# Kernel optimization log

Measured on AMD Instinct MI355X. Metric: run time of the kernel, lower is better.

The kernel has to match this reference:

```python
import jax, jax.numpy as jnp
import numpy as np

B, N, NODE_IN, RAW_IN, COV, H = 4096, 128, 16, 128, 8, 64
BN_EPS = 1e-5


def setup_inputs() -> dict:
    key = jax.random.key(0)
    ks = jax.random.split(key, 24)
    rn = lambda k, s, sc=0.1: jax.random.normal(k, s, jnp.float32) * sc
    return {
        'x_str': jax.random.normal(ks[0], (B, N, NODE_IN), jnp.float32),
        'x_raw': jax.random.normal(ks[1], (B, RAW_IN), jnp.float32),
        'adj': jax.random.uniform(ks[2], (B, N, N), jnp.float32),
        'x_cov': jax.random.normal(ks[3], (B, COV), jnp.float32),
        'age': jax.random.uniform(ks[4], (B, 1), jnp.float32),
        'gc1_w': rn(ks[5], (NODE_IN, H)), 'gc1_b': jnp.zeros((H,), jnp.float32),
        'gc2_w': rn(ks[6], (H, H)), 'gc2_b': jnp.zeros((H,), jnp.float32),
        'bn_gamma': jnp.ones((N,), jnp.float32), 'bn_beta': jnp.zeros((N,), jnp.float32),
        'bn_mean': jnp.zeros((N,), jnp.float32), 'bn_var': jnp.ones((N,), jnp.float32),
        'attn_w': rn(ks[7], (H, 1)), 'attn_b': jnp.zeros((1,), jnp.float32),
        'na_w': rn(ks[8], (H, 1)), 'na_b': jnp.zeros((1,), jnp.float32),
        'beta_w1': rn(ks[9], (RAW_IN + COV + H, 64)), 'beta_b1': jnp.zeros((64,), jnp.float32),
        'beta_w2': rn(ks[10], (64, 1)), 'beta_b2': jnp.zeros((1,), jnp.float32),
        'af_w1': rn(ks[11], (H + RAW_IN, 32)), 'af_b1': jnp.zeros((32,), jnp.float32),
        'af_w2': rn(ks[12], (32, 1)), 'af_b2': jnp.zeros((1,), jnp.float32),
    }


def _gcn(x, adj, w, b):
    # A_hat = A + I; support = D^{-1/2} A_hat D^{-1/2} (diag matmuls as broadcasts)
    a_hat = adj + jnp.eye(N, dtype=adj.dtype)
    d_inv = jnp.sum(a_hat, axis=2) ** -0.5  # [B,N]
    d_inv = jnp.where(jnp.isinf(d_inv), 0.0, d_inv)
    support = d_inv[:, :, None] * a_hat * d_inv[:, None, :]  # [B,N,N]
    agg = jnp.einsum('bnm,bmf->bnf', support, x)
    return agg @ w + b


def reference(x_str, x_raw, adj, x_cov, age,
              gc1_w, gc1_b, gc2_w, gc2_b,
              bn_gamma, bn_beta, bn_mean, bn_var,
              attn_w, attn_b, na_w, na_b,
              beta_w1, beta_b1, beta_w2, beta_b2,
              af_w1, af_b1, af_w2, af_b2):
    h = jax.nn.elu(_gcn(x_str, adj, gc1_w, gc1_b))      # dropout = identity (eval)
    h = jax.nn.elu(_gcn(h, adj, gc2_w, gc2_b))
    # BatchNorm1d over channel dim N (eval mode, running stats)
    h = (h - bn_mean[None, :, None]) * jax.lax.rsqrt(bn_var + BN_EPS)[None, :, None]
    h = h * bn_gamma[None, :, None] + bn_beta[None, :, None]

    attn_scores = h @ attn_w + attn_b                   # [B,N,1]
    weights = jax.nn.softmax(attn_scores, axis=1)
    alpha_node = jax.nn.softplus(h @ na_w + na_b)       # [B,N,1]
    graph_emb = jnp.sum(h * weights, axis=1)            # [B,H]

    beta_in = jnp.concatenate([x_raw, x_cov, graph_emb], axis=1)
    beta = jax.nn.sigmoid(jnp.tanh(beta_in @ beta_w1 + beta_b1) @ beta_w2 + beta_b2)

    alpha_in = jnp.concatenate([graph_emb, x_raw], axis=1)
    decay_rate = jax.nn.softplus(jax.nn.relu(alpha_in @ af_w1 + af_b1) @ af_w2 + af_b2)

    pred = beta * (1.0 - decay_rate * age)
    return (pred, beta, decay_rate, alpha_node[..., 0], weights[..., 0])
```

## Files before the change

### kernel.cpp

```cpp
#include <hip/hip_runtime.h>
#include <hip/hip_bf16.h>
#include <math.h>

#define BB 4096
#define NN 128

typedef __attribute__((ext_vector_type(8))) __bf16 bf16x8;
typedef __attribute__((ext_vector_type(4))) __bf16 bf16x4;
typedef __attribute__((ext_vector_type(4))) float f32x4;

constexpr int OFF_XT   = 0;
constexpr int OFF_W1T  = 4352;
constexpr int OFF_AG1  = 9472;
constexpr int OFF_W2T  = 0;
constexpr int OFF_GEP  = 0;
constexpr int OFF_GP   = 2048;
constexpr int OFF_AP   = 4096;
constexpr int OFF_H1T  = 19712;
constexpr int OFF_AG2  = 19712;
constexpr int OFF_BNS  = 38144;
constexpr int OFF_BNB  = 38656;
constexpr int OFF_AW   = 39168;
constexpr int OFF_NW   = 39424;
constexpr int OFF_SCV  = 39680;
constexpr int OFF_GEV  = 40128;
constexpr int SMEM_BYTES = 40384;

__device__ inline float eluf(float x)      { return x > 0.f ? x : __expf(x) - 1.f; }
__device__ inline float softplusf(float x) { return (x > 20.f) ? x : log1pf(__expf(x)); }

__global__ __launch_bounds__(512, 8)
void agp_kernel(const float* __restrict__ x_str, const float* __restrict__ x_raw,
                const float* __restrict__ adj,   const float* __restrict__ x_cov,
                const float* __restrict__ age,
                const float* __restrict__ gc1_w, const float* __restrict__ gc1_b,
                const float* __restrict__ gc2_w, const float* __restrict__ gc2_b,
                const float* __restrict__ bn_gamma, const float* __restrict__ bn_beta,
                const float* __restrict__ bn_mean,  const float* __restrict__ bn_var,
                const float* __restrict__ attn_w, const float* __restrict__ attn_b,
                const float* __restrict__ na_w,   const float* __restrict__ na_b,
                const float* __restrict__ beta_w1, const float* __restrict__ beta_b1,
                const float* __restrict__ beta_w2, const float* __restrict__ beta_b2,
                const float* __restrict__ af_w1,  const float* __restrict__ af_b1,
                const float* __restrict__ af_w2,  const float* __restrict__ af_b2,
                float* __restrict__ out)
{
    extern __shared__ __align__(16) char smraw[];
    __bf16* XT  = (__bf16*)(smraw + OFF_XT);
    __bf16* W1T = (__bf16*)(smraw + OFF_W1T);
    __bf16* AG1 = (__bf16*)(smraw + OFF_AG1);
    __bf16* W2T = (__bf16*)(smraw + OFF_W2T);
    __bf16* H1T = (__bf16*)(smraw + OFF_H1T);
    float* GEp  = (float*)(smraw + OFF_GEP);
    float* GP   = (float*)(smraw + OFF_GP);
    float* AP   = (float*)(smraw + OFF_AP);
    float* BNS  = (float*)(smraw + OFF_BNS);
    float* BNB  = (float*)(smraw + OFF_BNB);
    float* AW   = (float*)(smraw + OFF_AW);
    float* NWv  = (float*)(smraw + OFF_NW);
    float* SCv  = (float*)(smraw + OFF_SCV);
    float* GEv  = (float*)(smraw + OFF_GEV);

    const int b = blockIdx.x;
    const int t = threadIdx.x;
    const int w    = t >> 6;
    const int lane = t & 63;
    const int ll = lane & 15;
    const int lh = lane >> 4;
    const int myrow = 16*w + ll;
    __bf16* AG2w = (__bf16*)(smraw + OFF_AG2) + w*1152;

    bf16x8 sf[4];
    float dr[4];
    float dm;
    {
        const float* arow = adj + (size_t)b*NN*NN + (size_t)myrow*NN;
        const bool hasd = (((myrow >> 3) & 3) == lh);
        const int  dkt  = myrow >> 5;
        const int  didx = myrow & 7;
        #pragma unroll
        for (int kt = 0; kt < 4; ++kt) {
            int c0 = kt*32 + 8*lh;
            float4 a  = *reinterpret_cast<const float4*>(arow + c0);
            float4 a2 = *reinterpret_cast<const float4*>(arow + c0 + 4);
            if (kt == dkt && hasd) {
                a.x  += (didx==0)?1.f:0.f; a.y  += (didx==1)?1.f:0.f;
                a.z  += (didx==2)?1.f:0.f; a.w  += (didx==3)?1.f:0.f;
                a2.x += (didx==4)?1.f:0.f; a2.y += (didx==5)?1.f:0.f;
                a2.z += (didx==6)?1.f:0.f; a2.w += (didx==7)?1.f:0.f;
            }
            bf16x8 s;
            s[0]=(__bf16)a.x;  s[1]=(__bf16)a.y;  s[2]=(__bf16)a.z;  s[3]=(__bf16)a.w;
            s[4]=(__bf16)a2.x; s[5]=(__bf16)a2.y; s[6]=(__bf16)a2.z; s[7]=(__bf16)a2.w;
            sf[kt] = s;
        }
        bf16x8 ones;
        #pragma unroll
        for (int i = 0; i < 8; ++i) ones[i] = (__bf16)1.0f;
        f32x4 rsacc = {0.f, 0.f, 0.f, 0.f};
        #pragma unroll
        for (int kt = 0; kt < 4; ++kt)
            rsacc = __builtin_amdgcn_mfma_f32_16x16x32_bf16(sf[kt], ones, rsacc, 0, 0, 0);
        #pragma unroll
        for (int r = 0; r < 4; ++r) dr[r] = rsqrtf(__shfl(rsacc[r], 16*lh));
        float tmp[4];
        #pragma unroll
        for (int r = 0; r < 4; ++r) tmp[r] = __shfl(rsacc[r], 16*(ll >> 2));
        float s01 = (ll & 1) ? tmp[1] : tmp[0];
        float s23 = (ll & 1) ? tmp[3] : tmp[2];
        dm = rsqrtf((ll & 2) ? s23 : s01);
    }
    {
        float4 xr = *reinterpret_cast<const float4*>(x_str + (size_t)b*NN*16 + myrow*16 + 4*lh);
        XT[(4*lh+0)*136 + myrow] = (__bf16)(xr.x * dm);
        XT[(4*lh+1)*136 + myrow] = (__bf16)(xr.y * dm);
        XT[(4*lh+2)*136 + myrow] = (__bf16)(xr.z * dm);
        XT[(4*lh+3)*136 + myrow] = (__bf16)(xr.w * dm);
    }
    if (t < 256) {
        int j = t & 63, k0 = (t >> 6) * 4;
        bf16x4 pk;
        pk[0] = (__bf16)gc1_w[(k0+0)*64 + j];
        pk[1] = (__bf16)gc1_w[(k0+1)*64 + j];
        pk[2] = (__bf16)gc1_w[(k0+2)*64 + j];
        pk[3] = (__bf16)gc1_w[(k0+3)*64 + j];
        *reinterpret_cast<bf16x4*>(&W1T[j*40 + k0]) = pk;
        bf16x4 z4; z4[0]=z4[1]=z4[2]=z4[3]=(__bf16)0.f;
        *reinterpret_cast<bf16x4*>(&W1T[(t>>2)*40 + 16 + (t&3)*4]) = z4;
    }
    {
        bf16x4 z4; z4[0]=z4[1]=z4[2]=z4[3]=(__bf16)0.f;
        *reinterpret_cast<bf16x4*>(&AG1[(t>>2)*40 + 16 + (t&3)*4]) = z4;
    }
    if (t < 128) {
        float g = bn_gamma[t], be = bn_beta[t], mu = bn_mean[t], va = bn_var[t];
        float sc = g * rsqrtf(va + 1e-5f);
        BNS[t] = sc;
        BNB[t] = be - mu*sc;
    } else if (t < 192) {
        AW[t-128] = attn_w[t-128];
    } else if (t < 256) {
        NWv[t-192] = na_w[t-192];
    }
    __syncthreads();

    {
        f32x4 acc = {0.f, 0.f, 0.f, 0.f};
        #pragma unroll
        for (int kt = 0; kt < 4; ++kt) {
            bf16x8 bf = *reinterpret_cast<const bf16x8*>(&XT[ll*136 + kt*32 + 8*lh]);
            acc = __builtin_amdgcn_mfma_f32_16x16x32_bf16(sf[kt], bf, acc, 0, 0, 0);
        }
        #pragma unroll
        for (int r = 0; r < 4; ++r)
            AG1[(16*w + 4*lh + r)*40 + ll] = (__bf16)(acc[r] * dr[r]);
    }

    {
        bf16x8 a = *reinterpret_cast<const bf16x8*>(&AG1[(16*w + ll)*40 + 8*lh]);
        #pragma unroll
        for (int jt = 0; jt < 4; ++jt) {
            bf16x8 bf = *reinterpret_cast<const bf16x8*>(&W1T[(16*jt + ll)*40 + 8*lh]);
            f32x4 z = {0.f, 0.f, 0.f, 0.f};
            f32x4 acc = __builtin_amdgcn_mfma_f32_16x16x32_bf16(a, bf, z, 0, 0, 0);
            float bj = gc1_b[16*jt + ll];
            bf16x4 pk;
            #pragma unroll
            for (int r = 0; r < 4; ++r)
                pk[r] = (__bf16)(eluf(acc[r] + bj) * dr[r]);
            *reinterpret_cast<bf16x4*>(&H1T[(16*jt + ll)*136 + 16*w + 4*lh]) = pk;
        }
    }
    __syncthreads();

    float w2r[8];
    {
        int j = t & 63, k0 = (t >> 6) * 8;
        #pragma unroll
        for (int i = 0; i < 8; ++i) w2r[i] = gc2_w[(k0 + i)*64 + j];
    }

    bf16x4 pk2[4];
    {
        f32x4 acc2[4];
        #pragma unroll
        for (int jt = 0; jt < 4; ++jt) acc2[jt] = (f32x4){0.f, 0.f, 0.f, 0.f};
        #pragma unroll
        for (int kt = 0; kt < 4; ++kt) {
            #pragma unroll
            for (int jt = 0; jt < 4; ++jt) {
                bf16x8 bf = *reinterpret_cast<const bf16x8*>(&H1T[(16*jt + ll)*136 + kt*32 + 8*lh]);
                acc2[jt] = __builtin_amdgcn_mfma_f32_16x16x32_bf16(sf[kt], bf, acc2[jt], 0, 0, 0);
            }
        }
        #pragma unroll
        for (int jt = 0; jt < 4; ++jt)
            #pragma unroll
            for (int r = 0; r < 4; ++r)
                pk2[jt][r] = (__bf16)(acc2[jt][r] * dr[r]);
    }
    {
        int j = t & 63, k0 = (t >> 6) * 8;
        bf16x8 pv;
        #pragma unroll
        for (int i = 0; i < 8; ++i) pv[i] = (__bf16)w2r[i];
        *reinterpret_cast<bf16x8*>(&W2T[j*72 + k0]) = pv;
    }
    __syncthreads();

    #pragma unroll
    for (int jt = 0; jt < 4; ++jt)
        #pragma unroll
        for (int r = 0; r < 4; ++r)
            AG2w[(4*lh + r)*72 + 16*jt + ll] = pk2[jt][r];

    f32x4 hv[4];
    {
        #pragma unroll
        for (int jt = 0; jt < 4; ++jt) hv[jt] = (f32x4){0.f, 0.f, 0.f, 0.f};
        #pragma unroll
        for (int kt = 0; kt < 2; ++kt) {
            bf16x8 a = *reinterpret_cast<const bf16x8*>(&AG2w[ll*72 + kt*32 + 8*lh]);
            #pragma unroll
            for (int jt = 0; jt < 4; ++jt) {
                bf16x8 bf = *reinterpret_cast<const bf16x8*>(&W2T[(16*jt + ll)*72 + kt*32 + 8*lh]);
                hv[jt] = __builtin_amdgcn_mfma_f32_16x16x32_bf16(a, bf, hv[jt], 0, 0, 0);
            }
        }
        #pragma unroll
        for (int jt = 0; jt < 4; ++jt) {
            float bj = gc2_b[16*jt + ll];
            #pragma unroll
            for (int r = 0; r < 4; ++r) {
                int row = 16*w + 4*lh + r;
                hv[jt][r] = eluf(hv[jt][r] + bj) * BNS[row] + BNB[row];
            }
        }
    }

    float scA[4];
    {
        float aA[4] = {0,0,0,0}, aN[4] = {0,0,0,0};
        #pragma unroll
        for (int jt = 0; jt < 4; ++jt) {
            float wA = AW[16*jt + ll], wN = NWv[16*jt + ll];
            #pragma unroll
            for (int r = 0; r < 4; ++r) {
                aA[r] += hv[jt][r] * wA;
                aN[r] += hv[jt][r] * wN;
            }
        }
        #pragma unroll
        for (int m = 1; m <= 8; m <<= 1) {
            #pragma unroll
            for (int r = 0; r < 4; ++r) {
                aA[r] += __shfl_xor(aA[r], m);
                aN[r] += __shfl_xor(aN[r], m);
            }
        }
        float sA = attn_b[0], sN = na_b[0];
        #pragma unroll
        for (int r = 0; r < 4; ++r) scA[r] = aA[r] + sA;
        if (ll == 0) {
            float4 an4;
            an4.x = softplusf(aN[0] + sN); an4.y = softplusf(aN[1] + sN);
            an4.z = softplusf(aN[2] + sN); an4.w = softplusf(aN[3] + sN);
            #pragma unroll
            for (int r = 0; r < 4; ++r) SCv[16*w + 4*lh + r] = scA[r];
            *reinterpret_cast<float4*>(&out[12288 + (size_t)b*NN + 16*w + 4*lh]) = an4;
        }
    }
    __syncthreads();

    {
        float s0 = SCv[lane], s1 = SCv[64 + lane];
        float mx = fmaxf(s0, s1);
        #pragma unroll
        for (int m = 32; m >= 1; m >>= 1) mx = fmaxf(mx, __shfl_xor(mx, m));
        float e0 = __expf(s0 - mx), e1 = __expf(s1 - mx);
        float sum = e0 + e1;
        #pragma unroll
        for (int m = 32; m >= 1; m >>= 1) sum += __shfl_xor(sum, m);
        float inv = 1.f / sum;
        float wt[4];
        #pragma unroll
        for (int r = 0; r < 4; ++r) wt[r] = __expf(scA[r] - mx) * inv;
        if (ll == 0) {
            float4 w4; w4.x = wt[0]; w4.y = wt[1]; w4.z = wt[2]; w4.w = wt[3];
            *reinterpret_cast<float4*>(&out[536576 + (size_t)b*NN + 16*w + 4*lh]) = w4;
        }
        float gg[4];
        #pragma unroll
        for (int jt = 0; jt < 4; ++jt) {
            float g = 0.f;
            #pragma unroll
            for (int r = 0; r < 4; ++r) g += hv[jt][r] * wt[r];
            g += __shfl_xor(g, 16);
            g += __shfl_xor(g, 32);
            gg[jt] = g;
        }
        float s01 = (lh & 1) ? gg[1] : gg[0];
        float s23 = (lh & 1) ? gg[3] : gg[2];
        GEp[w*64 + lane] = (lh & 2) ? s23 : s01;
    }
    __syncthreads();

    if (t < 64) {
        float ge = 0.f;
        #pragma unroll
        for (int g = 0; g < 8; ++g) ge += GEp[g*64 + t];
        GEv[t] = ge;
    }
    __syncthreads();

    {
        const float* xr = x_raw + (size_t)b*128;
        int j = t & 63;
        float p = 0.f;
        if (w < 5) {
            const float* bw = beta_w1 + (size_t)(w*25)*64 + j;
            const float* xx = xr + w*25;
            #pragma unroll
            for (int k = 0; k < 25; ++k) p += xx[k] * bw[k*64];
        } else if (w == 5) {
            const float* cv = x_cov + (size_t)b*8;
            #pragma unroll
            for (int k = 0; k < 3; ++k)  p += xr[125+k] * beta_w1[(125+k)*64 + j];
            #pragma unroll
            for (int k = 0; k < 8; ++k)  p += cv[k]     * beta_w1[(128+k)*64 + j];
            #pragma unroll
            for (int k = 0; k < 14; ++k) p += GEv[k]    * beta_w1[(136+k)*64 + j];
        } else if (w == 6) {
            #pragma unroll
            for (int k = 0; k < 25; ++k) p += GEv[14+k] * beta_w1[(150+k)*64 + j];
        } else {
            #pragma unroll
            for (int k = 0; k < 25; ++k) p += GEv[39+k] * beta_w1[(175+k)*64 + j];
        }
        GP[w*64 + j] = p;

        int j2 = t & 31, ch = t >> 5;
        float q = 0.f;
        if (ch < 5) {
            int i0 = ch*12;
            #pragma unroll
            for (int k = 0; k < 12; ++k) q += GEv[i0+k] * af_w1[(i0+k)*32 + j2];
        } else if (ch == 5) {
            #pragma unroll
            for (int k = 0; k < 4; ++k) q += GEv[60+k] * af_w1[(60+k)*32 + j2];
            #pragma unroll
            for (int k = 0; k < 8; ++k) q += xr[k]     * af_w1[(64+k)*32 + j2];
        } else {
            int i0 = ch*12 - 64;
            #pragma unroll
            for (int k = 0; k < 12; ++k) q += xr[i0+k] * af_w1[(i0+k+64)*32 + j2];
        }
        AP[ch*32 + j2] = q;
    }
    __syncthreads();

    if (w == 0) {
        float accB = beta_b1[lane];
        #pragma unroll
        for (int c = 0; c < 8; ++c) accB += GP[c*64 + lane];
        float pB = tanhf(accB) * beta_w2[lane];
        #pragma unroll
        for (int m = 32; m >= 1; m >>= 1) pB += __shfl_xor(pB, m);
        float bet = 1.f / (1.f + __expf(-(pB + beta_b2[0])));

        int u = lane & 31;
        float accA = af_b1[u];
        #pragma unroll
        for (int c = 0; c < 16; ++c) accA += AP[c*32 + u];
        float rA = fmaxf(accA, 0.f) * af_w2[u];
        #pragma unroll
        for (int m = 16; m >= 1; m >>= 1) rA += __shfl_xor(rA, m);
        float dec = softplusf(rA + af_b2[0]);

        if (lane == 0) {
            out[b]        = bet * (1.f - dec * age[b]);
            out[4096 + b] = bet;
            out[8192 + b] = dec;
        }
    }
}

extern "C" void kernel_launch(void* const* d_in, const int* in_sizes, int n_in,
                              void* d_out, int out_size, void* d_ws, size_t ws_size,
                              hipStream_t stream) {
    (void)in_sizes; (void)n_in; (void)out_size; (void)d_ws; (void)ws_size;
    const float* x_str   = (const float*)d_in[0];
    const float* x_raw   = (const float*)d_in[1];
    const float* adj     = (const float*)d_in[2];
    const float* x_cov   = (const float*)d_in[3];
    const float* age     = (const float*)d_in[4];
    const float* gc1_w   = (const float*)d_in[5];
    const float* gc1_b   = (const float*)d_in[6];
    const float* gc2_w   = (const float*)d_in[7];
    const float* gc2_b   = (const float*)d_in[8];
    const float* bn_g    = (const float*)d_in[9];
    const float* bn_b    = (const float*)d_in[10];
    const float* bn_m    = (const float*)d_in[11];
    const float* bn_v    = (const float*)d_in[12];
    const float* attn_w  = (const float*)d_in[13];
    const float* attn_b  = (const float*)d_in[14];
    const float* na_w    = (const float*)d_in[15];
    const float* na_b    = (const float*)d_in[16];
    const float* beta_w1 = (const float*)d_in[17];
    const float* beta_b1 = (const float*)d_in[18];
    const float* beta_w2 = (const float*)d_in[19];
    const float* beta_b2 = (const float*)d_in[20];
    const float* af_w1   = (const float*)d_in[21];
    const float* af_b1   = (const float*)d_in[22];
    const float* af_w2   = (const float*)d_in[23];
    const float* af_b2   = (const float*)d_in[24];
    float* out = (float*)d_out;

    (void)hipFuncSetAttribute((const void*)agp_kernel,
                              hipFuncAttributeMaxDynamicSharedMemorySize, SMEM_BYTES);
    agp_kernel<<<BB, 512, SMEM_BYTES, stream>>>(
        x_str, x_raw, adj, x_cov, age,
        gc1_w, gc1_b, gc2_w, gc2_b,
        bn_g, bn_b, bn_m, bn_v,
        attn_w, attn_b, na_w, na_b,
        beta_w1, beta_b1, beta_w2, beta_b2,
        af_w1, af_b1, af_w2, af_b2,
        out);
}
```

Before: 106.2 us.

## Process two batch graphs per block to amortize weight staging and syncs

Each 512-thread block now handles two batch elements instead of one. Both graphs' adjacency loads are issued up front, and the GCN weight tiles, BN params and attention vectors are staged once and held in registers for reuse across both graphs. Per-graph scratch buffers are doubled in shared memory. Launch bounds drop from 8 to 4 waves-per-EU and the grid halves, which raises register and LDS use per block and cuts the number of resident blocks.

```diff
diff --git a/kernel.cpp b/kernel.cpp
--- a/kernel.cpp
+++ b/kernel.cpp
@@ -9,27 +9,29 @@
 typedef __attribute__((ext_vector_type(4))) __bf16 bf16x4;
 typedef __attribute__((ext_vector_type(4))) float f32x4;
 
-constexpr int OFF_XT   = 0;
-constexpr int OFF_W1T  = 4352;
-constexpr int OFF_AG1  = 9472;
-constexpr int OFF_W2T  = 0;
-constexpr int OFF_GEP  = 0;
-constexpr int OFF_GP   = 2048;
-constexpr int OFF_AP   = 4096;
-constexpr int OFF_H1T  = 19712;
-constexpr int OFF_AG2  = 19712;
-constexpr int OFF_BNS  = 38144;
-constexpr int OFF_BNB  = 38656;
-constexpr int OFF_AW   = 39168;
-constexpr int OFF_NW   = 39424;
-constexpr int OFF_SCV  = 39680;
-constexpr int OFF_GEV  = 40128;
-constexpr int SMEM_BYTES = 40384;
+constexpr int OFF_W1T = 0;
+constexpr int OFF_W2T = 5120;
+constexpr int OFF_BNS = 14336;
+constexpr int OFF_BNB = 14848;
+constexpr int OFF_AW  = 15360;
+constexpr int OFF_NW  = 15616;
+constexpr int SHARED_END = 15872;
+constexpr int PB_SIZE = 32768;
+constexpr int PB_XT  = 0;
+constexpr int PB_AG1 = 4352;
+constexpr int PB_GEP = 0;
+constexpr int PB_GP  = 2048;
+constexpr int PB_AP  = 4096;
+constexpr int PB_H1T = 14592;
+constexpr int PB_AG2 = 14592;
+constexpr int PB_SCV = 32000;
+constexpr int PB_GEV = 32512;
+constexpr int SMEM_BYTES = SHARED_END + 2*PB_SIZE;
 
 __device__ inline float eluf(float x)      { return x > 0.f ? x : __expf(x) - 1.f; }
 __device__ inline float softplusf(float x) { return (x > 20.f) ? x : log1pf(__expf(x)); }
 
-__global__ __launch_bounds__(512, 8)
+__global__ __launch_bounds__(512, 4)
 void agp_kernel(const float* __restrict__ x_str, const float* __restrict__ x_raw,
                 const float* __restrict__ adj,   const float* __restrict__ x_cov,
                 const float* __restrict__ age,
@@ -46,35 +48,43 @@
                 float* __restrict__ out)
 {
     extern __shared__ __align__(16) char smraw[];
-    __bf16* XT  = (__bf16*)(smraw + OFF_XT);
     __bf16* W1T = (__bf16*)(smraw + OFF_W1T);
-    __bf16* AG1 = (__bf16*)(smraw + OFF_AG1);
     __bf16* W2T = (__bf16*)(smraw + OFF_W2T);
-    __bf16* H1T = (__bf16*)(smraw + OFF_H1T);
-    float* GEp  = (float*)(smraw + OFF_GEP);
-    float* GP   = (float*)(smraw + OFF_GP);
-    float* AP   = (float*)(smraw + OFF_AP);
     float* BNS  = (float*)(smraw + OFF_BNS);
     float* BNB  = (float*)(smraw + OFF_BNB);
     float* AW   = (float*)(smraw + OFF_AW);
     float* NWv  = (float*)(smraw + OFF_NW);
-    float* SCv  = (float*)(smraw + OFF_SCV);
-    float* GEv  = (float*)(smraw + OFF_GEV);
-
-    const int b = blockIdx.x;
+
+    const int b0 = blockIdx.x * 2;
     const int t = threadIdx.x;
     const int w    = t >> 6;
     const int lane = t & 63;
     const int ll = lane & 15;
     const int lh = lane >> 4;
     const int myrow = 16*w + ll;
-    __bf16* AG2w = (__bf16*)(smraw + OFF_AG2) + w*1152;
-
-    bf16x8 sf[4];
-    float dr[4];
-    float dm;
-    {
-        const float* arow = adj + (size_t)b*NN*NN + (size_t)myrow*NN;
+
+    char* PB0 = smraw + SHARED_END;
+    char* PB1 = smraw + SHARED_END + PB_SIZE;
+    __bf16* XTp[2]  = { (__bf16*)(PB0 + PB_XT),  (__bf16*)(PB1 + PB_XT)  };
+    __bf16* AG1p[2] = { (__bf16*)(PB0 + PB_AG1), (__bf16*)(PB1 + PB_AG1) };
+    __bf16* H1Tp[2] = { (__bf16*)(PB0 + PB_H1T), (__bf16*)(PB1 + PB_H1T) };
+    __bf16* AG2p[2] = { (__bf16*)(PB0 + PB_AG2) + w*1152, (__bf16*)(PB1 + PB_AG2) + w*1152 };
+    float* GEpp[2]  = { (float*)(PB0 + PB_GEP),  (float*)(PB1 + PB_GEP)  };
+    float* GPp[2]   = { (float*)(PB0 + PB_GP),   (float*)(PB1 + PB_GP)   };
+    float* APp[2]   = { (float*)(PB0 + PB_AP),   (float*)(PB1 + PB_AP)   };
+    float* SCvp[2]  = { (float*)(PB0 + PB_SCV),  (float*)(PB1 + PB_SCV)  };
+    float* GEvp[2]  = { (float*)(PB0 + PB_GEV),  (float*)(PB1 + PB_GEV)  };
+
+    bf16x8 sf[2][4];
+    float dr[2][4];
+    bf16x8 ones;
+    #pragma unroll
+    for (int i = 0; i < 8; ++i) ones[i] = (__bf16)1.0f;
+
+    #pragma unroll
+    for (int bb = 0; bb < 2; ++bb) {
+        const int bat = b0 + bb;
+        const float* arow = adj + (size_t)bat*NN*NN + (size_t)myrow*NN;
         const bool hasd = (((myrow >> 3) & 3) == lh);
         const int  dkt  = myrow >> 5;
         const int  didx = myrow & 7;
@@ -92,30 +102,25 @@
             bf16x8 s;
             s[0]=(__bf16)a.x;  s[1]=(__bf16)a.y;  s[2]=(__bf16)a.z;  s[3]=(__bf16)a.w;
             s[4]=(__bf16)a2.x; s[5]=(__bf16)a2.y; s[6]=(__bf16)a2.z; s[7]=(__bf16)a2.w;
-            sf[kt] = s;
-        }
-        bf16x8 ones;
-        #pragma unroll
-        for (int i = 0; i < 8; ++i) ones[i] = (__bf16)1.0f;
+            sf[bb][kt] = s;
+        }
         f32x4 rsacc = {0.f, 0.f, 0.f, 0.f};
         #pragma unroll
         for (int kt = 0; kt < 4; ++kt)
-            rsacc = __builtin_amdgcn_mfma_f32_16x16x32_bf16(sf[kt], ones, rsacc, 0, 0, 0);
-        #pragma unroll
-        for (int r = 0; r < 4; ++r) dr[r] = rsqrtf(__shfl(rsacc[r], 16*lh));
+            rsacc = __builtin_amdgcn_mfma_f32_16x16x32_bf16(sf[bb][kt], ones, rsacc, 0, 0, 0);
+        #pragma unroll
+        for (int r = 0; r < 4; ++r) dr[bb][r] = rsqrtf(__shfl(rsacc[r], 16*lh));
         float tmp[4];
         #pragma unroll
         for (int r = 0; r < 4; ++r) tmp[r] = __shfl(rsacc[r], 16*(ll >> 2));
         float s01 = (ll & 1) ? tmp[1] : tmp[0];
         float s23 = (ll & 1) ? tmp[3] : tmp[2];
-        dm = rsqrtf((ll & 2) ? s23 : s01);
-    }
-    {
-        float4 xr = *reinterpret_cast<const float4*>(x_str + (size_t)b*NN*16 + myrow*16 + 4*lh);
-        XT[(4*lh+0)*136 + myrow] = (__bf16)(xr.x * dm);
-        XT[(4*lh+1)*136 + myrow] = (__bf16)(xr.y * dm);
-        XT[(4*lh+2)*136 + myrow] = (__bf16)(xr.z * dm);
-        XT[(4*lh+3)*136 + myrow] = (__bf16)(xr.w * dm);
+        float dm = rsqrtf((ll & 2) ? s23 : s01);
+        float4 xr = *reinterpret_cast<const float4*>(x_str + (size_t)bat*NN*16 + myrow*16 + 4*lh);
+        XTp[bb][(4*lh+0)*136 + myrow] = (__bf16)(xr.x * dm);
+        XTp[bb][(4*lh+1)*136 + myrow] = (__bf16)(xr.y * dm);
+        XTp[bb][(4*lh+2)*136 + myrow] = (__bf16)(xr.z * dm);
+        XTp[bb][(4*lh+3)*136 + myrow] = (__bf16)(xr.w * dm);
     }
     if (t < 256) {
         int j = t & 63, k0 = (t >> 6) * 4;
@@ -130,7 +135,8 @@
     }
     {
         bf16x4 z4; z4[0]=z4[1]=z4[2]=z4[3]=(__bf16)0.f;
-        *reinterpret_cast<bf16x4*>(&AG1[(t>>2)*40 + 16 + (t&3)*4]) = z4;
+        *reinterpret_cast<bf16x4*>(&AG1p[0][(t>>2)*40 + 16 + (t&3)*4]) = z4;
+        *reinterpret_cast<bf16x4*>(&AG1p[1][(t>>2)*40 + 16 + (t&3)*4]) = z4;
     }
     if (t < 128) {
         float g = bn_gamma[t], be = bn_beta[t], mu = bn_mean[t], va = bn_var[t];
@@ -144,60 +150,68 @@
     }
     __syncthreads();
 
-    {
+    #pragma unroll
+    for (int bb = 0; bb < 2; ++bb) {
         f32x4 acc = {0.f, 0.f, 0.f, 0.f};
         #pragma unroll
         for (int kt = 0; kt < 4; ++kt) {
-            bf16x8 bf = *reinterpret_cast<const bf16x8*>(&XT[ll*136 + kt*32 + 8*lh]);
-            acc = __builtin_amdgcn_mfma_f32_16x16x32_bf16(sf[kt], bf, acc, 0, 0, 0);
+            bf16x8 bf = *reinterpret_cast<const bf16x8*>(&XTp[bb][ll*136 + kt*32 + 8*lh]);
+            acc = __builtin_amdgcn_mfma_f32_16x16x32_bf16(sf[bb][kt], bf, acc, 0, 0, 0);
         }
         #pragma unroll
         for (int r = 0; r < 4; ++r)
-            AG1[(16*w + 4*lh + r)*40 + ll] = (__bf16)(acc[r] * dr[r]);
-    }
-
-    {
-        bf16x8 a = *reinterpret_cast<const bf16x8*>(&AG1[(16*w + ll)*40 + 8*lh]);
-        #pragma unroll
-        for (int jt = 0; jt < 4; ++jt) {
-            bf16x8 bf = *reinterpret_cast<const bf16x8*>(&W1T[(16*jt + ll)*40 + 8*lh]);
-            f32x4 z = {0.f, 0.f, 0.f, 0.f};
-            f32x4 acc = __builtin_amdgcn_mfma_f32_16x16x32_bf16(a, bf, z, 0, 0, 0);
-            float bj = gc1_b[16*jt + ll];
-            bf16x4 pk;
+            AG1p[bb][(16*w + 4*lh + r)*40 + ll] = (__bf16)(acc[r] * dr[bb][r]);
+    }
+
+    {
+        bf16x8 w1f[4];
+        #pragma unroll
+        for (int jt = 0; jt < 4; ++jt)
+            w1f[jt] = *reinterpret_cast<const bf16x8*>(&W1T[(16*jt + ll)*40 + 8*lh]);
+        #pragma unroll
+        for (int bb = 0; bb < 2; ++bb) {
+            bf16x8 a = *reinterpret_cast<const bf16x8*>(&AG1p[bb][(16*w + ll)*40 + 8*lh]);
+            #pragma unroll
+            for (int jt = 0; jt < 4; ++jt) {
+                f32x4 z = {0.f, 0.f, 0.f, 0.f};
+                f32x4 acc = __builtin_amdgcn_mfma_f32_16x16x32_bf16(a, w1f[jt], z, 0, 0, 0);
+                float bj = gc1_b[16*jt + ll];
+                bf16x4 pk;
+                #pragma unroll
+                for (int r = 0; r < 4; ++r)
+                    pk[r] = (__bf16)(eluf(acc[r] + bj) * dr[bb][r]);
+                *reinterpret_cast<bf16x4*>(&H1Tp[bb][(16*jt + ll)*136 + 16*w + 4*lh]) = pk;
+            }
+        }
+    }
+    __syncthreads();
+
+    float w2r[8];
+    {
+        int j = t & 63, k0 = (t >> 6) * 8;
+        #pragma unroll
+        for (int i = 0; i < 8; ++i) w2r[i] = gc2_w[(k0 + i)*64 + j];
+    }
+
+    bf16x4 pk2[2][4];
+    #pragma unroll
+    for (int bb = 0; bb < 2; ++bb) {
+        f32x4 acc2[4];
+        #pragma unroll
+        for (int jt = 0; jt < 4; ++jt) acc2[jt] = (f32x4){0.f, 0.f, 0.f, 0.f};
+        #pragma unroll
+        for (int kt = 0; kt < 4; ++kt) {
+            #pragma unroll
+            for (int jt = 0; jt < 4; ++jt) {
+                bf16x8 bf = *reinterpret_cast<const bf16x8*>(&H1Tp[bb][(16*jt + ll)*136 + kt*32 + 8*lh]);
+                acc2[jt] = __builtin_amdgcn_mfma_f32_16x16x32_bf16(sf[bb][kt], bf, acc2[jt], 0, 0, 0);
+            }
+        }
+        #pragma unroll
+        for (int jt = 0; jt < 4; ++jt)
             #pragma unroll
             for (int r = 0; r < 4; ++r)
-                pk[r] = (__bf16)(eluf(acc[r] + bj) * dr[r]);
-            *reinterpret_cast<bf16x4*>(&H1T[(16*jt + ll)*136 + 16*w + 4*lh]) = pk;
-        }
-    }
-    __syncthreads();
-
-    float w2r[8];
-    {
-        int j = t & 63, k0 = (t >> 6) * 8;
-        #pragma unroll
-        for (int i = 0; i < 8; ++i) w2r[i] = gc2_w[(k0 + i)*64 + j];
-    }
-
-    bf16x4 pk2[4];
-    {
-        f32x4 acc2[4];
-        #pragma unroll
-        for (int jt = 0; jt < 4; ++jt) acc2[jt] = (f32x4){0.f, 0.f, 0.f, 0.f};
-        #pragma unroll
-        for (int kt = 0; kt < 4; ++kt) {
-            #pragma unroll
-            for (int jt = 0; jt < 4; ++jt) {
-                bf16x8 bf = *reinterpret_cast<const bf16x8*>(&H1T[(16*jt + ll)*136 + kt*32 + 8*lh]);
-                acc2[jt] = __builtin_amdgcn_mfma_f32_16x16x32_bf16(sf[kt], bf, acc2[jt], 0, 0, 0);
-            }
-        }
-        #pragma unroll
-        for (int jt = 0; jt < 4; ++jt)
-            #pragma unroll
-            for (int r = 0; r < 4; ++r)
-                pk2[jt][r] = (__bf16)(acc2[jt][r] * dr[r]);
+                pk2[bb][jt][r] = (__bf16)(acc2[jt][r] * dr[bb][r]);
     }
     {
         int j = t & 63, k0 = (t >> 6) * 8;
@@ -209,71 +223,91 @@
     __syncthreads();
 
     #pragma unroll
-    for (int jt = 0; jt < 4; ++jt)
-        #pragma unroll
-        for (int r = 0; r < 4; ++r)
-            AG2w[(4*lh + r)*72 + 16*jt + ll] = pk2[jt][r];
-
-    f32x4 hv[4];
-    {
-        #pragma unroll
-        for (int jt = 0; jt < 4; ++jt) hv[jt] = (f32x4){0.f, 0.f, 0.f, 0.f};
-        #pragma unroll
-        for (int kt = 0; kt < 2; ++kt) {
-            bf16x8 a = *reinterpret_cast<const bf16x8*>(&AG2w[ll*72 + kt*32 + 8*lh]);
+    for (int bb = 0; bb < 2; ++bb)
+        #pragma unroll
+        for (int jt = 0; jt < 4; ++jt)
+            #pragma unroll
+            for (int r = 0; r < 4; ++r)
+                AG2p[bb][(4*lh + r)*72 + 16*jt + ll] = pk2[bb][jt][r];
+
+    f32x4 hv[2][4];
+    {
+        bf16x8 w2f[2][4];
+        #pragma unroll
+        for (int kt = 0; kt < 2; ++kt)
+            #pragma unroll
+            for (int jt = 0; jt < 4; ++jt)
+                w2f[kt][jt] = *reinterpret_cast<const bf16x8*>(&W2T[(16*jt + ll)*72 + kt*32 + 8*lh]);
+        float bns[4], bnb_[4], bj2[4];
+        #pragma unroll
+        for (int r = 0; r < 4; ++r) {
+            int row = 16*w + 4*lh + r;
+            bns[r] = BNS[row]; bnb_[r] = BNB[row];
+        }
+        #pragma unroll
+        for (int jt = 0; jt < 4; ++jt) bj2[jt] = gc2_b[16*jt + ll];
+        #pragma unroll
+        for (int bb = 0; bb < 2; ++bb) {
+            #pragma unroll
+            for (int jt = 0; jt < 4; ++jt) hv[bb][jt] = (f32x4){0.f, 0.f, 0.f, 0.f};
+            #pragma unroll
+            for (int kt = 0; kt < 2; ++kt) {
+                bf16x8 a = *reinterpret_cast<const bf16x8*>(&AG2p[bb][ll*72 + kt*32 + 8*lh]);
+                #pragma unroll
+                for (int jt = 0; jt < 4; ++jt)
+                    hv[bb][jt] = __builtin_amdgcn_mfma_f32_16x16x32_bf16(a, w2f[kt][jt], hv[bb][jt], 0, 0, 0);
+            }
+            #pragma unroll
+            for (int jt = 0; jt < 4; ++jt)
+                #pragma unroll
+                for (int r = 0; r < 4; ++r)
+                    hv[bb][jt][r] = eluf(hv[bb][jt][r] + bj2[jt]) * bns[r] + bnb_[r];
+        }
+    }
+
+    float scA[2][4];
+    {
+        float wA[4], wN[4];
+        #pragma unroll
+        for (int jt = 0; jt < 4; ++jt) { wA[jt] = AW[16*jt + ll]; wN[jt] = NWv[16*jt + ll]; }
+        float sA = attn_b[0], sN = na_b[0];
+        #pragma unroll
+        for (int bb = 0; bb < 2; ++bb) {
+            float aA[4] = {0,0,0,0}, aN[4] = {0,0,0,0};
             #pragma unroll
             for (int jt = 0; jt < 4; ++jt) {
-                bf16x8 bf = *reinterpret_cast<const bf16x8*>(&W2T[(16*jt + ll)*72 + kt*32 + 8*lh]);
-                hv[jt] = __builtin_amdgcn_mfma_f32_16x16x32_bf16(a, bf, hv[jt], 0, 0, 0);
-            }
-        }
-        #pragma unroll
-        for (int jt = 0; jt < 4; ++jt) {
-            float bj = gc2_b[16*jt + ll];
-            #pragma unroll
-            for (int r = 0; r < 4; ++r) {
-                int row = 16*w + 4*lh + r;
-                hv[jt][r] = eluf(hv[jt][r] + bj) * BNS[row] + BNB[row];
-            }
-        }
-    }
-
-    float scA[4];
-    {
-        float aA[4] = {0,0,0,0}, aN[4] = {0,0,0,0};
-        #pragma unroll
-        for (int jt = 0; jt < 4; ++jt) {
-            float wA = AW[16*jt + ll], wN = NWv[16*jt + ll];
-            #pragma unroll
-            for (int r = 0; r < 4; ++r) {
-                aA[r] += hv[jt][r] * wA;
-                aN[r] += hv[jt][r] * wN;
-            }
-        }
-        #pragma unroll
-        for (int m = 1; m <= 8; m <<= 1) {
-            #pragma unroll
-            for (int r = 0; r < 4; ++r) {
-                aA[r] += __shfl_xor(aA[r], m);
-                aN[r] += __shfl_xor(aN[r], m);
-            }
-        }
-        float sA = attn_b[0], sN = na_b[0];
-        #pragma unroll
-        for (int r = 0; r < 4; ++r) scA[r] = aA[r] + sA;
-        if (ll == 0) {
-            float4 an4;
-            an4.x = softplusf(aN[0] + sN); an4.y = softplusf(aN[1] + sN);
-            an4.z = softplusf(aN[2] + sN); an4.w = softplusf(aN[3] + sN);
-            #pragma unroll
-            for (int r = 0; r < 4; ++r) SCv[16*w + 4*lh + r] = scA[r];
-            *reinterpret_cast<float4*>(&out[12288 + (size_t)b*NN + 16*w + 4*lh]) = an4;
-        }
-    }
-    __syncthreads();
-
-    {
-        float s0 = SCv[lane], s1 = SCv[64 + lane];
+                #pragma unroll
+                for (int r = 0; r < 4; ++r) {
+                    aA[r] += hv[bb][jt][r] * wA[jt];
+                    aN[r] += hv[bb][jt][r] * wN[jt];
+                }
+            }
+            #pragma unroll
+            for (int m = 1; m <= 8; m <<= 1) {
+                #pragma unroll
+                for (int r = 0; r < 4; ++r) {
+                    aA[r] += __shfl_xor(aA[r], m);
+                    aN[r] += __shfl_xor(aN[r], m);
+                }
+            }
+            #pragma unroll
+            for (int r = 0; r < 4; ++r) scA[bb][r] = aA[r] + sA;
+            if (ll == 0) {
+                int bat = b0 + bb;
+                float4 an4;
+                an4.x = softplusf(aN[0] + sN); an4.y = softplusf(aN[1] + sN);
+                an4.z = softplusf(aN[2] + sN); an4.w = softplusf(aN[3] + sN);
+                #pragma unroll
+                for (int r = 0; r < 4; ++r) SCvp[bb][16*w + 4*lh + r] = scA[bb][r];
+                *reinterpret_cast<float4*>(&out[12288 + (size_t)bat*NN + 16*w + 4*lh]) = an4;
+            }
+        }
+    }
+    __syncthreads();
+
+    #pragma unroll
+    for (int bb = 0; bb < 2; ++bb) {
+        float s0 = SCvp[bb][lane], s1 = SCvp[bb][64 + lane];
         float mx = fmaxf(s0, s1);
         #pragma unroll
         for (int m = 32; m >= 1; m >>= 1) mx = fmaxf(mx, __shfl_xor(mx, m));
@@ -284,37 +318,42 @@
         float inv = 1.f / sum;
         float wt[4];
         #pragma unroll
-        for (int r = 0; r < 4; ++r) wt[r] = __expf(scA[r] - mx) * inv;
+        for (int r = 0; r < 4; ++r) wt[r] = __expf(scA[bb][r] - mx) * inv;
         if (ll == 0) {
+            int bat = b0 + bb;
             float4 w4; w4.x = wt[0]; w4.y = wt[1]; w4.z = wt[2]; w4.w = wt[3];
-            *reinterpret_cast<float4*>(&out[536576 + (size_t)b*NN + 16*w + 4*lh]) = w4;
+            *reinterpret_cast<float4*>(&out[536576 + (size_t)bat*NN + 16*w + 4*lh]) = w4;
         }
         float gg[4];
         #pragma unroll
         for (int jt = 0; jt < 4; ++jt) {
             float g = 0.f;
             #pragma unroll
-            for (int r = 0; r < 4; ++r) g += hv[jt][r] * wt[r];
+            for (int r = 0; r < 4; ++r) g += hv[bb][jt][r] * wt[r];
             g += __shfl_xor(g, 16);
             g += __shfl_xor(g, 32);
             gg[jt] = g;
         }
         float s01 = (lh & 1) ? gg[1] : gg[0];
         float s23 = (lh & 1) ? gg[3] : gg[2];
-        GEp[w*64 + lane] = (lh & 2) ? s23 : s01;
-    }
-    __syncthreads();
-
-    if (t < 64) {
+        GEpp[bb][w*64 + lane] = (lh & 2) ? s23 : s01;
+    }
+    __syncthreads();
+
+    if (t < 128) {
+        int bb = t >> 6, j = t & 63;
         float ge = 0.f;
         #pragma unroll
-        for (int g = 0; g < 8; ++g) ge += GEp[g*64 + t];
-        GEv[t] = ge;
-    }
-    __syncthreads();
-
-    {
-        const float* xr = x_raw + (size_t)b*128;
+        for (int g = 0; g < 8; ++g) ge += GEpp[bb][g*64 + j];
+        GEvp[bb][j] = ge;
+    }
+    __syncthreads();
+
+    #pragma unroll
+    for (int bb = 0; bb < 2; ++bb) {
+        int bat = b0 + bb;
+        const float* xr = x_raw + (size_t)bat*128;
+        const float* GEv = GEvp[bb];
         int j = t & 63;
         float p = 0.f;
         if (w < 5) {
@@ -323,7 +362,7 @@
             #pragma unroll
             for (int k = 0; k < 25; ++k) p += xx[k] * bw[k*64];
         } else if (w == 5) {
-            const float* cv = x_cov + (size_t)b*8;
+            const float* cv = x_cov + (size_t)bat*8;
             #pragma unroll
             for (int k = 0; k < 3; ++k)  p += xr[125+k] * beta_w1[(125+k)*64 + j];
             #pragma unroll
@@ -337,7 +376,7 @@
             #pragma unroll
             for (int k = 0; k < 25; ++k) p += GEv[39+k] * beta_w1[(175+k)*64 + j];
         }
-        GP[w*64 + j] = p;
+        GPp[bb][w*64 + j] = p;
 
         int j2 = t & 31, ch = t >> 5;
         float q = 0.f;
@@ -355,14 +394,16 @@
             #pragma unroll
             for (int k = 0; k < 12; ++k) q += xr[i0+k] * af_w1[(i0+k+64)*32 + j2];
         }
-        AP[ch*32 + j2] = q;
-    }
-    __syncthreads();
-
-    if (w == 0) {
+        APp[bb][ch*32 + j2] = q;
+    }
+    __syncthreads();
+
+    if (w < 2) {
+        const int bb = w;
+        const int bat = b0 + bb;
         float accB = beta_b1[lane];
         #pragma unroll
-        for (int c = 0; c < 8; ++c) accB += GP[c*64 + lane];
+        for (int c = 0; c < 8; ++c) accB += GPp[bb][c*64 + lane];
         float pB = tanhf(accB) * beta_w2[lane];
         #pragma unroll
         for (int m = 32; m >= 1; m >>= 1) pB += __shfl_xor(pB, m);
@@ -371,16 +412,16 @@
         int u = lane & 31;
         float accA = af_b1[u];
         #pragma unroll
-        for (int c = 0; c < 16; ++c) accA += AP[c*32 + u];
+        for (int c = 0; c < 16; ++c) accA += APp[bb][c*32 + u];
         float rA = fmaxf(accA, 0.f) * af_w2[u];
         #pragma unroll
         for (int m = 16; m >= 1; m >>= 1) rA += __shfl_xor(rA, m);
         float dec = softplusf(rA + af_b2[0]);
 
         if (lane == 0) {
-            out[b]        = bet * (1.f - dec * age[b]);
-            out[4096 + b] = bet;
-            out[8192 + b] = dec;
+            out[bat]        = bet * (1.f - dec * age[bat]);
+            out[4096 + bat] = bet;
+            out[8192 + bat] = dec;
         }
     }
 }
@@ -418,7 +459,7 @@
 
     (void)hipFuncSetAttribute((const void*)agp_kernel,
                               hipFuncAttributeMaxDynamicSharedMemorySize, SMEM_BYTES);
-    agp_kernel<<<BB, 512, SMEM_BYTES, stream>>>(
+    agp_kernel<<<BB/2, 512, SMEM_BYTES, stream>>>(
         x_str, x_raw, adj, x_cov, age,
         gc1_w, gc1_b, gc2_w, gc2_b,
         bn_g, bn_b, bn_m, bn_v,
```

Result: slower. 119.9 us (+12.9%).
